# Optimization experiments

Hardware: AMD Instinct MI355X
Metric: run time of the kernel (lower is better)

The kernel has to match this reference:

```python
import jax, jax.numpy as jnp
import numpy as np
from jax import lax

B, C = 16, 1024          # batch, in_channels (= spectral length)
N_HEAD = 8
N_FEAT = 512
CH = N_FEAT // N_HEAD    # 64 per-head channels
EPS = 1e-5


def setup_inputs() -> dict:
    key = jax.random.key(0)
    ks = jax.random.split(key, 9)
    x = jax.random.normal(ks[0], (B, C), dtype=jnp.float32)
    # BatchNorm1d (inference mode) params / running stats
    bn_gamma = jax.random.normal(ks[1], (C,), dtype=jnp.float32) * 0.1 + 1.0
    bn_beta = jax.random.normal(ks[2], (C,), dtype=jnp.float32) * 0.1
    bn_mean = jax.random.normal(ks[3], (C,), dtype=jnp.float32) * 0.1
    bn_var = jax.random.uniform(ks[4], (C,), dtype=jnp.float32, minval=0.5, maxval=1.5)
    # in_conv: Conv1d(1, 3*N_FEAT, kernel=3, stride=1, pad=1) -> weight [O, I, K]
    w_in = jax.random.normal(ks[5], (3 * N_FEAT, 1, 3), dtype=jnp.float32) * (1.0 / np.sqrt(3))
    b_in = jax.random.normal(ks[6], (3 * N_FEAT,), dtype=jnp.float32) * 0.02
    # proj_h: Conv1d(N_FEAT, 1, kernel=1). zero_module zeros it at init; use
    # nonzero values so the reference exercises the full graph (trained state).
    w_out = jax.random.normal(ks[7], (1, N_FEAT, 1), dtype=jnp.float32) * (1.0 / np.sqrt(N_FEAT))
    b_out = jax.random.normal(ks[8], (1,), dtype=jnp.float32) * 0.02
    return {"x": x, "bn_gamma": bn_gamma, "bn_beta": bn_beta, "bn_mean": bn_mean,
            "bn_var": bn_var, "w_in": w_in, "b_in": b_in, "w_out": w_out, "b_out": b_out}


def reference(x, bn_gamma, bn_beta, bn_mean, bn_var, w_in, b_in, w_out, b_out):
    b, c = x.shape
    # BatchNorm1d on [b, c] input (eval mode, per-channel stats)
    xn = (x - bn_mean) * jax.lax.rsqrt(bn_var + EPS) * bn_gamma + bn_beta
    x1 = xn[:, None, :]  # [b, 1, c]
    # Conv1d(1 -> 3*N_FEAT, k=3, pad=1)
    qkv = lax.conv_general_dilated(
        x1, w_in, window_strides=(1,), padding=((1, 1),),
        dimension_numbers=("NCH", "OIH", "NCH")) + b_in[None, :, None]  # [b, 3F, c]
    # QKVAttentionLegacy: reshape to [b*H, 3*ch, c], split, scaled dot-product
    qkv = qkv.reshape(b * N_HEAD, 3 * CH, c)
    q, k, v = jnp.split(qkv, 3, axis=1)          # each [b*H, ch, c]
    scale = CH ** -0.25
    w = jnp.einsum("bct,bcs->bts", q * scale, k * scale)  # [b*H, c, c]
    w = jax.nn.softmax(w, axis=-1)
    a = jnp.einsum("bts,bcs->bct", w, v)          # [b*H, ch, c]
    h = a.reshape(b, N_FEAT, c)
    # proj_h: 1x1 conv N_FEAT -> 1
    h = jnp.einsum("of,bft->bot", w_out[:, :, 0][None].squeeze(0)[None].squeeze(0)[None] if False else w_out[:, :, 0], h) + b_out[None, :, None]  # [b, 1, c]
    return (h + x1).reshape(b, c)
```

## Files before the change

kernel.cpp:

```cpp
#include <hip/hip_runtime.h>
#include <hip/hip_bf16.h>
#include <math.h>

#define NB 16
#define SEQ 1024
#define NHEAD 8
#define CHD 64
#define NBH (NB*NHEAD)

typedef __attribute__((ext_vector_type(8))) short short8v;
typedef __attribute__((ext_vector_type(4))) float f32x4;

#define OFF_QT  0u
#define OFF_KT  (OFF_QT + 16777216u)
#define OFF_VP  (OFF_KT + 16777216u)

__device__ __forceinline__ short f2bf_raw(float f) {
  union { float f; unsigned u; } un; un.f = f;
  unsigned r = un.u + 0x7fffu + ((un.u >> 16) & 1u);
  return (short)(r >> 16);
}

__device__ __forceinline__ void load_lds16(const void* g, void* l) {
  __builtin_amdgcn_global_load_lds(
      (const __attribute__((address_space(1))) void*)g,
      (__attribute__((address_space(3))) void*)l, 16, 0, 0);
}

__global__ void __launch_bounds__(256) k_prep(
    const float* __restrict__ x, const float* __restrict__ gam,
    const float* __restrict__ be, const float* __restrict__ mu,
    const float* __restrict__ va, const float* __restrict__ w_in,
    const float* __restrict__ b_in, const float* __restrict__ w_out,
    const float* __restrict__ b_out,
    short* __restrict__ qT, short* __restrict__ kT,
    float* __restrict__ vp, float* __restrict__ out) {
  __shared__ float xns[264];
  __shared__ float wpack[192][4];
  __shared__ float hcs[4];
  int bid = blockIdx.x;
  int tc = bid & 3, h = (bid >> 2) & 7, b = bid >> 5;
  int tid = threadIdx.x;
  if (tid < 192) {
    int o = h * 192 + tid;
    wpack[tid][0] = w_in[o*3]; wpack[tid][1] = w_in[o*3+1];
    wpack[tid][2] = w_in[o*3+2]; wpack[tid][3] = b_in[o];
  }
  int t0 = tc * 256;
  {
    int tg = t0 + tid;
    float xv = (x[b*SEQ+tg] - mu[tg]) * rsqrtf(va[tg]+1e-5f) * gam[tg] + be[tg];
    xns[tid + 1] = xv;
    if (h == 0) out[b*SEQ + tg] = xv + b_out[0];
    if (tid == 0) {
      int tm = t0 - 1;
      xns[0] = (tm >= 0) ?
        (x[b*SEQ+tm] - mu[tm]) * rsqrtf(va[tm]+1e-5f) * gam[tm] + be[tm] : 0.f;
    }
    if (tid == 255) {
      int tp = t0 + 256;
      xns[257] = (tp < SEQ) ?
        (x[b*SEQ+tp] - mu[tp]) * rsqrtf(va[tp]+1e-5f) * gam[tp] + be[tp] : 0.f;
    }
  }
  __syncthreads();
  if (tid < 4) {
    float s = 0.f;
    for (int c = 0; c < CHD; ++c) s += w_out[h*CHD + c] * wpack[128 + c][tid];
    hcs[tid] = s;
  }
  __syncthreads();

  int bh = b * NHEAD + h;
  vp[bh*SEQ + t0 + tid] =
      hcs[0]*xns[tid] + hcs[1]*xns[tid+1] + hcs[2]*xns[tid+2] + hcs[3];

  const float QS = 0.125f * 1.4426950408889634f;
  int c_oct = tid & 7, tgrp = tid >> 3;
  long tbase = ((long)bh * SEQ + t0 + tgrp*8);
  #pragma unroll
  for (int i = 0; i < 8; ++i) {
    int tl = tgrp*8 + i;
    float xm = xns[tl], x0 = xns[tl+1], xp = xns[tl+2];
    short8v pq, pk;
    #pragma unroll
    for (int u = 0; u < 8; ++u) {
      int c = c_oct*8 + u;
      float4 wq = *(const float4*)wpack[c];
      float4 wk = *(const float4*)wpack[64 + c];
      pq[u] = f2bf_raw((wq.x*xm + wq.y*x0 + wq.z*xp + wq.w) * QS);
      pk[u] = f2bf_raw(wk.x*xm + wk.y*x0 + wk.z*xp + wk.w);
    }
    *(short8v*)(qT + (tbase + i)*CHD + c_oct*8) = pq;
    *(short8v*)(kT + (tbase + i)*CHD + c_oct*8) = pk;
  }
}

#define UPD2(ssv, ddv, e0, e1, vv0, vv1) { \
  float p0 = __builtin_amdgcn_exp2f(e0); \
  float p1 = __builtin_amdgcn_exp2f(e1); \
  ssv += p0 + p1; \
  ddv = fmaf(p0, (vv0), fmaf(p1, (vv1), ddv)); }

__global__ void __launch_bounds__(256) k_attn(const short* __restrict__ qT,
                                              const short* __restrict__ kT,
                                              const float* __restrict__ vp,
                                              float* __restrict__ out) {
  __shared__ char kbuf[8192];
  __shared__ float vbuf[SEQ];
  int bid = blockIdx.x;
  int bh = bid & 127;
  int ttile = bid >> 7;
  int tid = threadIdx.x;
  int wv = tid >> 6, lane = tid & 63;
  int l15 = lane & 15, g = lane >> 4;

  const short* qbase = qT + (long)bh * SEQ * CHD;
  const short* kbase = kT + (long)bh * SEQ * CHD;

  int gidx = wv * 64 + lane;
  int sr = gidx >> 3, sj = gidx & 7;
  int ksrcoff = sr * 128 + ((sj ^ (sr & 7)) * 16);

  load_lds16((const char*)(vp + bh*SEQ) + gidx*16, (char*)vbuf + wv*1024);

  int trow0 = ttile * 128 + wv * 32;
  short8v aA0 = *(const short8v*)(qbase + (trow0 +      l15)*CHD + g*8);
  short8v aB0 = *(const short8v*)(qbase + (trow0 +      l15)*CHD + 32 + g*8);
  short8v aA1 = *(const short8v*)(qbase + (trow0 + 16 + l15)*CHD + g*8);
  short8v aB1 = *(const short8v*)(qbase + (trow0 + 16 + l15)*CHD + 32 + g*8);

  int ra = l15*128 + ((g       ^ (l15 & 7)) * 16);
  int rb = l15*128 + (((g ^ 4) ^ (l15 & 7)) * 16);

  float s0[4], d0[4], s1[4], d1[4];
  #pragma unroll
  for (int r = 0; r < 4; ++r) { s0[r]=0.f; s1[r]=0.f; d0[r]=0.f; d1[r]=0.f; }

#define STAGEK(CIDX, BOFF) \
  load_lds16((const char*)kbase + (CIDX)*4096 + ksrcoff, kbuf + (BOFF) + wv*1024);

#define COMPUTE(BOFF, CB) { \
  f32x4 acc00, acc01, acc10, acc11; \
  { short8v b0 = *(const short8v*)(kbuf + (BOFF) + ra); \
    short8v b1 = *(const short8v*)(kbuf + (BOFF) + rb); \
    acc00 = __builtin_amdgcn_mfma_f32_16x16x32_bf16(aA0, b0, (f32x4){0,0,0,0}, 0,0,0); \
    acc00 = __builtin_amdgcn_mfma_f32_16x16x32_bf16(aB0, b1, acc00, 0,0,0); \
    acc01 = __builtin_amdgcn_mfma_f32_16x16x32_bf16(aA1, b0, (f32x4){0,0,0,0}, 0,0,0); \
    acc01 = __builtin_amdgcn_mfma_f32_16x16x32_bf16(aB1, b1, acc01, 0,0,0); } \
  { short8v b0 = *(const short8v*)(kbuf + (BOFF) + 2048 + ra); \
    short8v b1 = *(const short8v*)(kbuf + (BOFF) + 2048 + rb); \
    acc10 = __builtin_amdgcn_mfma_f32_16x16x32_bf16(aA0, b0, (f32x4){0,0,0,0}, 0,0,0); \
    acc10 = __builtin_amdgcn_mfma_f32_16x16x32_bf16(aB0, b1, acc10, 0,0,0); \
    acc11 = __builtin_amdgcn_mfma_f32_16x16x32_bf16(aA1, b0, (f32x4){0,0,0,0}, 0,0,0); \
    acc11 = __builtin_amdgcn_mfma_f32_16x16x32_bf16(aB1, b1, acc11, 0,0,0); } \
  float vv0 = vbuf[(CB) + l15], vv1 = vbuf[(CB) + 16 + l15]; \
  _Pragma("unroll") \
  for (int r = 0; r < 4; ++r) { \
    UPD2(s0[r], d0[r], acc00[r], acc10[r], vv0, vv1); \
    UPD2(s1[r], d1[r], acc01[r], acc11[r], vv0, vv1); \
  } }

  STAGEK(0, 0);
  __syncthreads();
  #pragma unroll 1
  for (int c = 0; c < 32; c += 2) {
    STAGEK(c + 1, 4096);
    COMPUTE(0, c * 32);
    __syncthreads();
    if (c + 2 < 32) STAGEK(c + 2, 0);
    COMPUTE(4096, (c + 1) * 32);
    __syncthreads();
  }

  #pragma unroll
  for (int r = 0; r < 4; ++r) {
    #pragma unroll
    for (int mk = 1; mk < 16; mk <<= 1) {
      s0[r] += __shfl_xor(s0[r], mk); d0[r] += __shfl_xor(d0[r], mk);
      s1[r] += __shfl_xor(s1[r], mk); d1[r] += __shfl_xor(d1[r], mk);
    }
  }

  if (l15 == 0) {
    int b = bh >> 3;
    #pragma unroll
    for (int r = 0; r < 4; ++r) {
      atomicAdd(&out[b*SEQ + trow0 +      g*4 + r], d0[r] / s0[r]);
      atomicAdd(&out[b*SEQ + trow0 + 16 + g*4 + r], d1[r] / s1[r]);
    }
  }
}

extern "C" void kernel_launch(void* const* d_in, const int* in_sizes, int n_in,
                              void* d_out, int out_size, void* d_ws, size_t ws_size,
                              hipStream_t stream) {
  const float* x   = (const float*)d_in[0];
  const float* g   = (const float*)d_in[1];
  const float* be  = (const float*)d_in[2];
  const float* mu  = (const float*)d_in[3];
  const float* va  = (const float*)d_in[4];
  const float* win = (const float*)d_in[5];
  const float* bin = (const float*)d_in[6];
  const float* wo  = (const float*)d_in[7];
  const float* bo  = (const float*)d_in[8];
  float* out = (float*)d_out;

  char* ws = (char*)d_ws;
  short* qT = (short*)(ws + OFF_QT);
  short* kT = (short*)(ws + OFF_KT);
  float* vpj = (float*)(ws + OFF_VP);

  hipLaunchKernelGGL(k_prep, dim3(512), dim3(256), 0, stream,
                     x, g, be, mu, va, win, bin, wo, bo, qT, kT, vpj, out);
  hipLaunchKernelGGL(k_attn, dim3(NBH * 8), dim3(256), 0, stream, qT, kT, vpj, out);
}
```

Before: 119.7 us.

## Use per-wave private K double buffers and drop block barriers in attention loop

The attention kernel now gives each wave its own double-buffered LDS copy of every K chunk. Each wave stages the whole chunk itself with async global-to-LDS loads and waits on vmcnt instead of calling __syncthreads every iteration. This removes block-wide barrier stalls and lets waves run independently. In exchange it costs four times the K load traffic from L2 per block and more LDS. The prep kernel also hoists the conv weights from LDS into registers before the output loop.

```diff
diff --git a/kernel.cpp b/kernel.cpp
--- a/kernel.cpp
+++ b/kernel.cpp
@@ -69,6 +69,14 @@
     for (int c = 0; c < CHD; ++c) s += w_out[h*CHD + c] * wpack[128 + c][tid];
     hcs[tid] = s;
   }
+
+  int c_oct = tid & 7, tgrp = tid >> 3;
+  float4 rq[8], rk[8];
+  #pragma unroll
+  for (int u = 0; u < 8; ++u) {
+    rq[u] = *(const float4*)wpack[c_oct*8 + u];
+    rk[u] = *(const float4*)wpack[64 + c_oct*8 + u];
+  }
   __syncthreads();
 
   int bh = b * NHEAD + h;
@@ -76,7 +84,6 @@
       hcs[0]*xns[tid] + hcs[1]*xns[tid+1] + hcs[2]*xns[tid+2] + hcs[3];
 
   const float QS = 0.125f * 1.4426950408889634f;
-  int c_oct = tid & 7, tgrp = tid >> 3;
   long tbase = ((long)bh * SEQ + t0 + tgrp*8);
   #pragma unroll
   for (int i = 0; i < 8; ++i) {
@@ -85,11 +92,8 @@
     short8v pq, pk;
     #pragma unroll
     for (int u = 0; u < 8; ++u) {
-      int c = c_oct*8 + u;
-      float4 wq = *(const float4*)wpack[c];
-      float4 wk = *(const float4*)wpack[64 + c];
-      pq[u] = f2bf_raw((wq.x*xm + wq.y*x0 + wq.z*xp + wq.w) * QS);
-      pk[u] = f2bf_raw(wk.x*xm + wk.y*x0 + wk.z*xp + wk.w);
+      pq[u] = f2bf_raw((rq[u].x*xm + rq[u].y*x0 + rq[u].z*xp + rq[u].w) * QS);
+      pk[u] = f2bf_raw(rk[u].x*xm + rk[u].y*x0 + rk[u].z*xp + rk[u].w);
     }
     *(short8v*)(qT + (tbase + i)*CHD + c_oct*8) = pq;
     *(short8v*)(kT + (tbase + i)*CHD + c_oct*8) = pk;
@@ -106,7 +110,7 @@
                                               const short* __restrict__ kT,
                                               const float* __restrict__ vp,
                                               float* __restrict__ out) {
-  __shared__ char kbuf[8192];
+  __shared__ char kbuf[4][2][4096];
   __shared__ float vbuf[SEQ];
   int bid = blockIdx.x;
   int bh = bid & 127;
@@ -118,11 +122,18 @@
   const short* qbase = qT + (long)bh * SEQ * CHD;
   const short* kbase = kT + (long)bh * SEQ * CHD;
 
-  int gidx = wv * 64 + lane;
-  int sr = gidx >> 3, sj = gidx & 7;
-  int ksrcoff = sr * 128 + ((sj ^ (sr & 7)) * 16);
-
-  load_lds16((const char*)(vp + bh*SEQ) + gidx*16, (char*)vbuf + wv*1024);
+  int base_swz = (lane >> 3) * 128 + (((lane & 7) ^ ((lane >> 3) & 7)) * 16);
+
+  load_lds16((const char*)(vp + bh*SEQ) + (wv*64 + lane)*16,
+             (char*)vbuf + wv*1024);
+
+#define STAGEW(CIDX, DBUF) { \
+  const char* sp_ = (const char*)kbase + (CIDX)*4096 + base_swz; \
+  char* dp_ = &kbuf[wv][DBUF][0]; \
+  load_lds16(sp_ +    0, dp_ +    0); \
+  load_lds16(sp_ + 1024, dp_ + 1024); \
+  load_lds16(sp_ + 2048, dp_ + 2048); \
+  load_lds16(sp_ + 3072, dp_ + 3072); }
 
   int trow0 = ttile * 128 + wv * 32;
   short8v aA0 = *(const short8v*)(qbase + (trow0 +      l15)*CHD + g*8);
@@ -130,6 +141,9 @@
   short8v aA1 = *(const short8v*)(qbase + (trow0 + 16 + l15)*CHD + g*8);
   short8v aB1 = *(const short8v*)(qbase + (trow0 + 16 + l15)*CHD + 32 + g*8);
 
+  STAGEW(0, 0);
+  STAGEW(1, 1);
+
   int ra = l15*128 + ((g       ^ (l15 & 7)) * 16);
   int rb = l15*128 + (((g ^ 4) ^ (l15 & 7)) * 16);
 
@@ -137,19 +151,17 @@
   #pragma unroll
   for (int r = 0; r < 4; ++r) { s0[r]=0.f; s1[r]=0.f; d0[r]=0.f; d1[r]=0.f; }
 
-#define STAGEK(CIDX, BOFF) \
-  load_lds16((const char*)kbase + (CIDX)*4096 + ksrcoff, kbuf + (BOFF) + wv*1024);
-
-#define COMPUTE(BOFF, CB) { \
+#define COMPUTE(DBUF, CB) { \
+  const char* kb = &kbuf[wv][DBUF][0]; \
   f32x4 acc00, acc01, acc10, acc11; \
-  { short8v b0 = *(const short8v*)(kbuf + (BOFF) + ra); \
-    short8v b1 = *(const short8v*)(kbuf + (BOFF) + rb); \
+  { short8v b0 = *(const short8v*)(kb + ra); \
+    short8v b1 = *(const short8v*)(kb + rb); \
     acc00 = __builtin_amdgcn_mfma_f32_16x16x32_bf16(aA0, b0, (f32x4){0,0,0,0}, 0,0,0); \
     acc00 = __builtin_amdgcn_mfma_f32_16x16x32_bf16(aB0, b1, acc00, 0,0,0); \
     acc01 = __builtin_amdgcn_mfma_f32_16x16x32_bf16(aA1, b0, (f32x4){0,0,0,0}, 0,0,0); \
     acc01 = __builtin_amdgcn_mfma_f32_16x16x32_bf16(aB1, b1, acc01, 0,0,0); } \
-  { short8v b0 = *(const short8v*)(kbuf + (BOFF) + 2048 + ra); \
-    short8v b1 = *(const short8v*)(kbuf + (BOFF) + 2048 + rb); \
+  { short8v b0 = *(const short8v*)(kb + 2048 + ra); \
+    short8v b1 = *(const short8v*)(kb + 2048 + rb); \
     acc10 = __builtin_amdgcn_mfma_f32_16x16x32_bf16(aA0, b0, (f32x4){0,0,0,0}, 0,0,0); \
     acc10 = __builtin_amdgcn_mfma_f32_16x16x32_bf16(aB0, b1, acc10, 0,0,0); \
     acc11 = __builtin_amdgcn_mfma_f32_16x16x32_bf16(aA1, b0, (f32x4){0,0,0,0}, 0,0,0); \
@@ -161,17 +173,17 @@
     UPD2(s1[r], d1[r], acc01[r], acc11[r], vv0, vv1); \
   } }
 
-  STAGEK(0, 0);
   __syncthreads();
+
   #pragma unroll 1
-  for (int c = 0; c < 32; c += 2) {
-    STAGEK(c + 1, 4096);
-    COMPUTE(0, c * 32);
-    __syncthreads();
-    if (c + 2 < 32) STAGEK(c + 2, 0);
-    COMPUTE(4096, (c + 1) * 32);
-    __syncthreads();
-  }
+  for (int c = 0; c < 31; ++c) {
+    asm volatile("s_waitcnt vmcnt(4)" ::: "memory");
+    COMPUTE(c & 1, c * 32);
+    asm volatile("" ::: "memory");
+    if (c + 2 < 32) STAGEW(c + 2, c & 1);
+  }
+  asm volatile("s_waitcnt vmcnt(0)" ::: "memory");
+  COMPUTE(1, 31 * 32);
 
   #pragma unroll
   for (int r = 0; r < 4; ++r) {
```

Result: faster. 117.0 us (-2.3%).
